# Kernel tuning notes

Hardware: AMD Instinct MI355X
Metric: run time of the kernel (lower is better)

The kernel has to match this reference:

```python
import jax, jax.numpy as jnp
import numpy as np

H = 16
EXPAND = 4
D_MLP = EXPAND * H
EPS = 1e-5


def setup_inputs() -> dict:
    key = jax.random.key(0)
    kx, k1, k2, k3, k4 = jax.random.split(key, 5)
    B, T = 128, 8192
    x = jax.random.normal(kx, (B, T, H), dtype=jnp.float32)
    # LayerNorm params
    ln_gamma = jnp.ones((H,), dtype=jnp.float32)
    ln_beta = jnp.zeros((H,), dtype=jnp.float32)
    # Linear params (PyTorch default init style: uniform in +-1/sqrt(fan_in))
    w1 = jax.random.uniform(k1, (D_MLP, H), minval=-1.0, maxval=1.0, dtype=jnp.float32) / np.sqrt(H)
    b1 = jax.random.uniform(k2, (D_MLP,), minval=-1.0, maxval=1.0, dtype=jnp.float32) / np.sqrt(H)
    w2 = jax.random.uniform(k3, (H, D_MLP), minval=-1.0, maxval=1.0, dtype=jnp.float32) / np.sqrt(D_MLP)
    b2 = jax.random.uniform(k4, (H,), minval=-1.0, maxval=1.0, dtype=jnp.float32) / np.sqrt(D_MLP)
    return {"x": x, "ln_gamma": ln_gamma, "ln_beta": ln_beta,
            "w1": w1, "b1": b1, "w2": w2, "b2": b2}


def reference(x, ln_gamma, ln_beta, w1, b1, w2, b2):
    # LayerNorm over last dim (eps=1e-5, elementwise affine)
    mean = jnp.mean(x, axis=-1, keepdims=True)
    var = jnp.mean(jnp.square(x - mean), axis=-1, keepdims=True)
    y = (x - mean) * jax.lax.rsqrt(var + EPS) * ln_gamma + ln_beta
    # fc1 -> ReLU -> fc2
    h = jax.nn.relu(jnp.einsum('bth,dh->btd', y, w1) + b1)  # (B, T, D_MLP)
    out = jnp.einsum('btd,hd->bth', h, w2) + b2             # (B, T, H)
    return x + out
```

## Files before the change

### kernel.cpp

```cpp
#include <hip/hip_runtime.h>
#include <hip/hip_bf16.h>


constexpr int H = 16;
constexpr int D = 64;
constexpr int BT = 256;
constexpr int XROW = 20;
constexpr int W1R = 40;
constexpr int W2R = 72;

typedef __attribute__((ext_vector_type(8))) short  short8;
typedef __attribute__((ext_vector_type(4))) float  floatx4;
typedef __attribute__((ext_vector_type(4))) unsigned uintx4;

__device__ inline unsigned short f2bf(float f) {
    __hip_bfloat16 h = __float2bfloat16(f);
    unsigned short u; __builtin_memcpy(&u, &h, 2); return u;
}
__device__ inline unsigned pk2(float a, float b) {
    __hip_bfloat162 h = __float22bfloat162_rn(make_float2(a, b));
    unsigned u; __builtin_memcpy(&u, &h, 4); return u;
}
__device__ inline floatx4 relu4(floatx4 v) {
    v.x = fmaxf(v.x, 0.f); v.y = fmaxf(v.y, 0.f);
    v.z = fmaxf(v.z, 0.f); v.w = fmaxf(v.w, 0.f);
    return v;
}

__global__ __launch_bounds__(256, 5) void ffn_kernel(
    const float* __restrict__ x,
    const float* __restrict__ ln_g,
    const float* __restrict__ ln_b,
    const float* __restrict__ w1,
    const float* __restrict__ b1,
    const float* __restrict__ w2,
    const float* __restrict__ b2,
    float* __restrict__ out,
    int ntok)
{
    __shared__ __align__(16) float          s_x[BT * XROW];
    __shared__ __align__(16) unsigned short s_w1h[D * W1R];
    __shared__ __align__(16) unsigned short s_w2h[H * W2R];
    __shared__ __align__(16) float          s_b2[H];

    const int tid = threadIdx.x;
    const int w = tid >> 6, l = tid & 63;
    const int li = l & 15, q = l >> 4;

    const size_t gbase = (size_t)(blockIdx.x * BT + w * 64) * H;
    floatx4 xin[4];
    #pragma unroll
    for (int r = 0; r < 4; r++)
        xin[r] = *(const floatx4*)(x + gbase + (r * 64 + l) * 4);

    for (int i = tid; i < D * 32; i += 256) {
        int d = i >> 5, k = i & 31;
        float v = (k < H) ? w1[d * H + k] : (k == H ? b1[d] : 0.f);
        s_w1h[d * W1R + k] = f2bf(v);
    }
    for (int i = tid; i < H * D; i += 256) {
        int c = i >> 6, k = i & 63;
        int dk = (k & 32) | (((k >> 2) & 1) << 4) | (((k >> 3) & 3) << 2) | (k & 3);
        s_w2h[c * W2R + k] = f2bf(w2[c * D + dk]);
    }
    if (tid < H) s_b2[tid] = b2[tid];

    #pragma unroll
    for (int r = 0; r < 4; r++) {
        int fi = (r * 64 + l) * 4, tt = fi >> 4, e = fi & 15;
        *(floatx4*)&s_x[(w * 64 + tt) * XROW + e] = xin[r];
    }
    __syncthreads();

    short8 a1[4];
    #pragma unroll
    for (int mt = 0; mt < 4; mt++)
        a1[mt] = *(const short8*)&s_w1h[(16 * mt + li) * W1R + q * 8];
    short8 a2[2];
    #pragma unroll
    for (int kt = 0; kt < 2; kt++)
        a2[kt] = *(const short8*)&s_w2h[li * W2R + kt * 32 + q * 8];
    floatx4 c2 = *(const floatx4*)&s_b2[4 * q];

    const int k0 = (q & 1) * 8;
    floatx4 ga = *(const floatx4*)(ln_g + k0);
    floatx4 gb = *(const floatx4*)(ln_g + k0 + 4);
    floatx4 ea = *(const floatx4*)(ln_b + k0);
    floatx4 eb = *(const floatx4*)(ln_b + k0 + 4);

    #pragma unroll
    for (int nt = 0; nt < 4; nt++) {
        float* xr = &s_x[(w * 64 + nt * 16 + li) * XROW];
        floatx4 xa = *(const floatx4*)(xr + k0);
        floatx4 xb = *(const floatx4*)(xr + k0 + 4);

        float ps = (xa.x + xa.y) + (xa.z + xa.w) + (xb.x + xb.y) + (xb.z + xb.w);
        float pq = 0.f;
        pq = fmaf(xa.x, xa.x, pq); pq = fmaf(xa.y, xa.y, pq);
        pq = fmaf(xa.z, xa.z, pq); pq = fmaf(xa.w, xa.w, pq);
        pq = fmaf(xb.x, xb.x, pq); pq = fmaf(xb.y, xb.y, pq);
        pq = fmaf(xb.z, xb.z, pq); pq = fmaf(xb.w, xb.w, pq);
        ps += __shfl_xor(ps, 16);
        pq += __shfl_xor(pq, 16);
        const float mean = ps * (1.0f / H);
        const float var  = fmaf(-mean, mean, pq * (1.0f / H));
        const float inv  = rsqrtf(var + 1e-5f);
        const float sa = inv, sb = -mean * inv;

        float y0 = fmaf(fmaf(xa.x, sa, sb), ga.x, ea.x);
        float y1 = fmaf(fmaf(xa.y, sa, sb), ga.y, ea.y);
        float y2 = fmaf(fmaf(xa.z, sa, sb), ga.z, ea.z);
        float y3 = fmaf(fmaf(xa.w, sa, sb), ga.w, ea.w);
        float y4 = fmaf(fmaf(xb.x, sa, sb), gb.x, eb.x);
        float y5 = fmaf(fmaf(xb.y, sa, sb), gb.y, eb.y);
        float y6 = fmaf(fmaf(xb.z, sa, sb), gb.z, eb.z);
        float y7 = fmaf(fmaf(xb.w, sa, sb), gb.w, eb.w);

        unsigned p0 = pk2(y0, y1), p1 = pk2(y2, y3),
                 p2 = pk2(y4, y5), p3 = pk2(y6, y7);
        if (q >= 2) { p0 = (q == 2) ? 0x3F80u : 0u; p1 = 0u; p2 = 0u; p3 = 0u; }
        uintx4 byu = { p0, p1, p2, p3 };
        short8 by; __builtin_memcpy(&by, &byu, 16);

        const floatx4 z = { 0.f, 0.f, 0.f, 0.f };
        floatx4 h0 = relu4(__builtin_amdgcn_mfma_f32_16x16x32_bf16(a1[0], by, z, 0, 0, 0));
        floatx4 h1 = relu4(__builtin_amdgcn_mfma_f32_16x16x32_bf16(a1[1], by, z, 0, 0, 0));
        floatx4 h2 = relu4(__builtin_amdgcn_mfma_f32_16x16x32_bf16(a1[2], by, z, 0, 0, 0));
        floatx4 h3 = relu4(__builtin_amdgcn_mfma_f32_16x16x32_bf16(a1[3], by, z, 0, 0, 0));

        uintx4 bh0u = { pk2(h0.x, h0.y), pk2(h0.z, h0.w),
                        pk2(h1.x, h1.y), pk2(h1.z, h1.w) };
        uintx4 bh1u = { pk2(h2.x, h2.y), pk2(h2.z, h2.w),
                        pk2(h3.x, h3.y), pk2(h3.z, h3.w) };
        short8 bh0, bh1;
        __builtin_memcpy(&bh0, &bh0u, 16);
        __builtin_memcpy(&bh1, &bh1u, 16);

        floatx4 o = __builtin_amdgcn_mfma_f32_16x16x32_bf16(a2[0], bh0, c2, 0, 0, 0);
        o = __builtin_amdgcn_mfma_f32_16x16x32_bf16(a2[1], bh1, o, 0, 0, 0);

        floatx4 xres = *(const floatx4*)(xr + 4 * q);
        o += xres;
        *(floatx4*)(xr + 4 * q) = o;
    }

    #pragma unroll
    for (int r = 0; r < 4; r++) {
        int fi = (r * 64 + l) * 4, tt = fi >> 4, e = fi & 15;
        *(floatx4*)(out + gbase + fi) = *(const floatx4*)&s_x[(w * 64 + tt) * XROW + e];
    }
}

extern "C" void kernel_launch(void* const* d_in, const int* in_sizes, int n_in,
                              void* d_out, int out_size, void* d_ws, size_t ws_size,
                              hipStream_t stream) {
    const float* x   = (const float*)d_in[0];
    const float* g   = (const float*)d_in[1];
    const float* be  = (const float*)d_in[2];
    const float* w1  = (const float*)d_in[3];
    const float* b1  = (const float*)d_in[4];
    const float* w2  = (const float*)d_in[5];
    const float* b2  = (const float*)d_in[6];
    float* out = (float*)d_out;
    const int ntok = in_sizes[0] / H;

    const int grid = ntok / BT;
    ffn_kernel<<<grid, 256, 0, stream>>>(x, g, be, w1, b1, w2, b2, out, ntok);
}
```

Measured before the change: 134.5 us.

## Remove shared-memory staging; load weights and activations directly into MFMA fragments

Drops the LDS staging of x, w1, w2 and b2 along with the __syncthreads. Each lane now packs weight fragments to bf16 straight from global memory, and reads x in the per-lane MFMA fragment layout. LayerNorm is computed once per 32-token pair, and the two 16-token halves are exchanged with a lane shuffle so every lane's work is used. The next tile is prefetched, and results are written straight to global memory, where the store pattern is less coalesced (16-byte strided per lane). The residual is also re-read from global memory, which adds redundant x traffic that the L2 cache is expected to absorb.

```diff
diff --git a/kernel.cpp b/kernel.cpp
--- a/kernel.cpp
+++ b/kernel.cpp
@@ -2,21 +2,16 @@
 #include <hip/hip_bf16.h>
 
 
-constexpr int H = 16;
-constexpr int D = 64;
-constexpr int BT = 256;
-constexpr int XROW = 20;
-constexpr int W1R = 40;
-constexpr int W2R = 72;
+constexpr int H   = 16;
+constexpr int D   = 64;
+constexpr int TPI = 32;
+constexpr int NIT = 2;
+constexpr int BT  = 4 * TPI * NIT;
 
-typedef __attribute__((ext_vector_type(8))) short  short8;
-typedef __attribute__((ext_vector_type(4))) float  floatx4;
+typedef __attribute__((ext_vector_type(8))) short    short8;
+typedef __attribute__((ext_vector_type(4))) float    floatx4;
 typedef __attribute__((ext_vector_type(4))) unsigned uintx4;
 
-__device__ inline unsigned short f2bf(float f) {
-    __hip_bfloat16 h = __float2bfloat16(f);
-    unsigned short u; __builtin_memcpy(&u, &h, 2); return u;
-}
 __device__ inline unsigned pk2(float a, float b) {
     __hip_bfloat162 h = __float22bfloat162_rn(make_float2(a, b));
     unsigned u; __builtin_memcpy(&u, &h, 4); return u;
@@ -25,6 +20,23 @@
     v.x = fmaxf(v.x, 0.f); v.y = fmaxf(v.y, 0.f);
     v.z = fmaxf(v.z, 0.f); v.w = fmaxf(v.w, 0.f);
     return v;
+}
+
+__device__ inline floatx4 tile_ffn(const short8* a1, const short8* a2,
+                                   floatx4 c2, short8 by) {
+    const floatx4 z = {0.f, 0.f, 0.f, 0.f};
+    floatx4 h0 = relu4(__builtin_amdgcn_mfma_f32_16x16x32_bf16(a1[0], by, z, 0, 0, 0));
+    floatx4 h1 = relu4(__builtin_amdgcn_mfma_f32_16x16x32_bf16(a1[1], by, z, 0, 0, 0));
+    floatx4 h2 = relu4(__builtin_amdgcn_mfma_f32_16x16x32_bf16(a1[2], by, z, 0, 0, 0));
+    floatx4 h3 = relu4(__builtin_amdgcn_mfma_f32_16x16x32_bf16(a1[3], by, z, 0, 0, 0));
+    uintx4 r0 = { pk2(h0.x, h0.y), pk2(h0.z, h0.w), pk2(h1.x, h1.y), pk2(h1.z, h1.w) };
+    uintx4 r1 = { pk2(h2.x, h2.y), pk2(h2.z, h2.w), pk2(h3.x, h3.y), pk2(h3.z, h3.w) };
+    short8 bh0, bh1;
+    __builtin_memcpy(&bh0, &r0, 16);
+    __builtin_memcpy(&bh1, &r1, 16);
+    floatx4 o = __builtin_amdgcn_mfma_f32_16x16x32_bf16(a2[0], bh0, c2, 0, 0, 0);
+    o = __builtin_amdgcn_mfma_f32_16x16x32_bf16(a2[1], bh1, o, 0, 0, 0);
+    return o;
 }
 
 __global__ __launch_bounds__(256, 5) void ffn_kernel(
@@ -38,61 +50,59 @@
     float* __restrict__ out,
     int ntok)
 {
-    __shared__ __align__(16) float          s_x[BT * XROW];
-    __shared__ __align__(16) unsigned short s_w1h[D * W1R];
-    __shared__ __align__(16) unsigned short s_w2h[H * W2R];
-    __shared__ __align__(16) float          s_b2[H];
-
     const int tid = threadIdx.x;
     const int w = tid >> 6, l = tid & 63;
     const int li = l & 15, q = l >> 4;
-
-    const size_t gbase = (size_t)(blockIdx.x * BT + w * 64) * H;
-    floatx4 xin[4];
-    #pragma unroll
-    for (int r = 0; r < 4; r++)
-        xin[r] = *(const floatx4*)(x + gbase + (r * 64 + l) * 4);
-
-    for (int i = tid; i < D * 32; i += 256) {
-        int d = i >> 5, k = i & 31;
-        float v = (k < H) ? w1[d * H + k] : (k == H ? b1[d] : 0.f);
-        s_w1h[d * W1R + k] = f2bf(v);
-    }
-    for (int i = tid; i < H * D; i += 256) {
-        int c = i >> 6, k = i & 63;
-        int dk = (k & 32) | (((k >> 2) & 1) << 4) | (((k >> 3) & 3) << 2) | (k & 3);
-        s_w2h[c * W2R + k] = f2bf(w2[c * D + dk]);
-    }
-    if (tid < H) s_b2[tid] = b2[tid];
-
-    #pragma unroll
-    for (int r = 0; r < 4; r++) {
-        int fi = (r * 64 + l) * 4, tt = fi >> 4, e = fi & 15;
-        *(floatx4*)&s_x[(w * 64 + tt) * XROW + e] = xin[r];
-    }
-    __syncthreads();
+    const int hb = q >> 1;
+    const int k0 = (q & 1) * 8;
 
     short8 a1[4];
     #pragma unroll
-    for (int mt = 0; mt < 4; mt++)
-        a1[mt] = *(const short8*)&s_w1h[(16 * mt + li) * W1R + q * 8];
+    for (int mt = 0; mt < 4; mt++) {
+        const int d = 16 * mt + li;
+        uintx4 u = {0u, 0u, 0u, 0u};
+        if (q < 2) {
+            floatx4 wa = *(const floatx4*)(w1 + d * H + k0);
+            floatx4 wb = *(const floatx4*)(w1 + d * H + k0 + 4);
+            u.x = pk2(wa.x, wa.y); u.y = pk2(wa.z, wa.w);
+            u.z = pk2(wb.x, wb.y); u.w = pk2(wb.z, wb.w);
+        } else if (q == 2) {
+            u.x = pk2(b1[d], 0.f);
+        }
+        __builtin_memcpy(&a1[mt], &u, 16);
+    }
     short8 a2[2];
     #pragma unroll
-    for (int kt = 0; kt < 2; kt++)
-        a2[kt] = *(const short8*)&s_w2h[li * W2R + kt * 32 + q * 8];
-    floatx4 c2 = *(const floatx4*)&s_b2[4 * q];
+    for (int kt = 0; kt < 2; kt++) {
+        floatx4 wa = *(const floatx4*)(w2 + li * D + kt * 32 + 4 * q);
+        floatx4 wb = *(const floatx4*)(w2 + li * D + kt * 32 + 16 + 4 * q);
+        uintx4 u = { pk2(wa.x, wa.y), pk2(wa.z, wa.w), pk2(wb.x, wb.y), pk2(wb.z, wb.w) };
+        __builtin_memcpy(&a2[kt], &u, 16);
+    }
+    const floatx4 c2 = *(const floatx4*)(b2 + 4 * q);
+    const floatx4 ga = *(const floatx4*)(ln_g + k0);
+    const floatx4 gb = *(const floatx4*)(ln_g + k0 + 4);
+    const floatx4 ea = *(const floatx4*)(ln_b + k0);
+    const floatx4 eb = *(const floatx4*)(ln_b + k0 + 4);
 
-    const int k0 = (q & 1) * 8;
-    floatx4 ga = *(const floatx4*)(ln_g + k0);
-    floatx4 gb = *(const floatx4*)(ln_g + k0 + 4);
-    floatx4 ea = *(const floatx4*)(ln_b + k0);
-    floatx4 eb = *(const floatx4*)(ln_b + k0 + 4);
+    const int tok0 = blockIdx.x * BT + w * (TPI * NIT);
+    const float* xfrag = x + (size_t)(tok0 + hb * 16 + li) * H + k0;
+
+    floatx4 xa = *(const floatx4*)(xfrag);
+    floatx4 xb = *(const floatx4*)(xfrag + 4);
 
     #pragma unroll
-    for (int nt = 0; nt < 4; nt++) {
-        float* xr = &s_x[(w * 64 + nt * 16 + li) * XROW];
-        floatx4 xa = *(const floatx4*)(xr + k0);
-        floatx4 xb = *(const floatx4*)(xr + k0 + 4);
+    for (int it = 0; it < NIT; ++it) {
+        floatx4 na = xa, nb = xb;
+        if (it + 1 < NIT) {
+            const float* nx = xfrag + (size_t)(it + 1) * TPI * H;
+            na = *(const floatx4*)(nx);
+            nb = *(const floatx4*)(nx + 4);
+        }
+        const int base = tok0 + it * TPI;
+        const size_t rA = (size_t)(base + li) * H + 4 * q;
+        const floatx4 xrA = *(const floatx4*)(x + rA);
+        const floatx4 xrB = *(const floatx4*)(x + rA + 16 * H);
 
         float ps = (xa.x + xa.y) + (xa.z + xa.w) + (xb.x + xb.y) + (xb.z + xb.w);
         float pq = 0.f;
@@ -107,48 +117,38 @@
         const float inv  = rsqrtf(var + 1e-5f);
         const float sa = inv, sb = -mean * inv;
 
-        float y0 = fmaf(fmaf(xa.x, sa, sb), ga.x, ea.x);
-        float y1 = fmaf(fmaf(xa.y, sa, sb), ga.y, ea.y);
-        float y2 = fmaf(fmaf(xa.z, sa, sb), ga.z, ea.z);
-        float y3 = fmaf(fmaf(xa.w, sa, sb), ga.w, ea.w);
-        float y4 = fmaf(fmaf(xb.x, sa, sb), gb.x, eb.x);
-        float y5 = fmaf(fmaf(xb.y, sa, sb), gb.y, eb.y);
-        float y6 = fmaf(fmaf(xb.z, sa, sb), gb.z, eb.z);
-        float y7 = fmaf(fmaf(xb.w, sa, sb), gb.w, eb.w);
+        const float y0 = fmaf(fmaf(xa.x, sa, sb), ga.x, ea.x);
+        const float y1 = fmaf(fmaf(xa.y, sa, sb), ga.y, ea.y);
+        const float y2 = fmaf(fmaf(xa.z, sa, sb), ga.z, ea.z);
+        const float y3 = fmaf(fmaf(xa.w, sa, sb), ga.w, ea.w);
+        const float y4 = fmaf(fmaf(xb.x, sa, sb), gb.x, eb.x);
+        const float y5 = fmaf(fmaf(xb.y, sa, sb), gb.y, eb.y);
+        const float y6 = fmaf(fmaf(xb.z, sa, sb), gb.z, eb.z);
+        const float y7 = fmaf(fmaf(xb.w, sa, sb), gb.w, eb.w);
 
-        unsigned p0 = pk2(y0, y1), p1 = pk2(y2, y3),
-                 p2 = pk2(y4, y5), p3 = pk2(y6, y7);
-        if (q >= 2) { p0 = (q == 2) ? 0x3F80u : 0u; p1 = 0u; p2 = 0u; p3 = 0u; }
-        uintx4 byu = { p0, p1, p2, p3 };
-        short8 by; __builtin_memcpy(&by, &byu, 16);
+        const unsigned p0 = pk2(y0, y1), p1 = pk2(y2, y3),
+                       p2 = pk2(y4, y5), p3 = pk2(y6, y7);
+        const unsigned s0 = __shfl_xor(p0, 32), s1 = __shfl_xor(p1, 32),
+                       s2 = __shfl_xor(p2, 32), s3 = __shfl_xor(p3, 32);
 
-        const floatx4 z = { 0.f, 0.f, 0.f, 0.f };
-        floatx4 h0 = relu4(__builtin_amdgcn_mfma_f32_16x16x32_bf16(a1[0], by, z, 0, 0, 0));
-        floatx4 h1 = relu4(__builtin_amdgcn_mfma_f32_16x16x32_bf16(a1[1], by, z, 0, 0, 0));
-        floatx4 h2 = relu4(__builtin_amdgcn_mfma_f32_16x16x32_bf16(a1[2], by, z, 0, 0, 0));
-        floatx4 h3 = relu4(__builtin_amdgcn_mfma_f32_16x16x32_bf16(a1[3], by, z, 0, 0, 0));
+        const bool lo = (q < 2);
+        const unsigned cq2 = (q == 2) ? 0x3F80u : 0u;
+        uintx4 uA = { lo ? p0 : cq2, lo ? p1 : 0u, lo ? p2 : 0u, lo ? p3 : 0u };
+        uintx4 uB = { lo ? s0 : cq2, lo ? s1 : 0u, lo ? s2 : 0u, lo ? s3 : 0u };
+        short8 byA, byB;
+        __builtin_memcpy(&byA, &uA, 16);
+        __builtin_memcpy(&byB, &uB, 16);
 
-        uintx4 bh0u = { pk2(h0.x, h0.y), pk2(h0.z, h0.w),
-                        pk2(h1.x, h1.y), pk2(h1.z, h1.w) };
-        uintx4 bh1u = { pk2(h2.x, h2.y), pk2(h2.z, h2.w),
-                        pk2(h3.x, h3.y), pk2(h3.z, h3.w) };
-        short8 bh0, bh1;
-        __builtin_memcpy(&bh0, &bh0u, 16);
-        __builtin_memcpy(&bh1, &bh1u, 16);
+        floatx4 oA = tile_ffn(a1, a2, c2, byA);
+        oA += xrA;
+        *(floatx4*)(out + rA) = oA;
+        floatx4 oB = tile_ffn(a1, a2, c2, byB);
+        oB += xrB;
+        *(floatx4*)(out + rA + 16 * H) = oB;
 
-        floatx4 o = __builtin_amdgcn_mfma_f32_16x16x32_bf16(a2[0], bh0, c2, 0, 0, 0);
-        o = __builtin_amdgcn_mfma_f32_16x16x32_bf16(a2[1], bh1, o, 0, 0, 0);
-
-        floatx4 xres = *(const floatx4*)(xr + 4 * q);
-        o += xres;
-        *(floatx4*)(xr + 4 * q) = o;
+        xa = na; xb = nb;
     }
-
-    #pragma unroll
-    for (int r = 0; r < 4; r++) {
-        int fi = (r * 64 + l) * 4, tt = fi >> 4, e = fi & 15;
-        *(floatx4*)(out + gbase + fi) = *(const floatx4*)&s_x[(w * 64 + tt) * XROW + e];
-    }
+    (void)ntok;
 }
 
 extern "C" void kernel_launch(void* const* d_in, const int* in_sizes, int n_in,
```

Measured after the change: 136.5 us. Within noise of the previous version (+1.5%).
